# Kernel tuning notes

Measured on AMD Instinct MI355X. Metric: run time of the kernel, lower is better.

Reference implementation:

```python
import jax, jax.numpy as jnp
import numpy as np

DIM = 768
N_HEADS = 12
HEAD_DIM = DIM // N_HEADS
SCALE = HEAD_DIM ** -0.5


def setup_inputs() -> dict:
    key = jax.random.key(0)
    ks = jax.random.split(key, 5)
    B, N = 8, 1024
    x = jax.random.normal(ks[0], (B, N, DIM), dtype=jnp.float32)
    # Linear weights stored as (in, out) for x @ W; torch stores (out, in).
    w_qkv = jax.random.normal(ks[1], (DIM, 3 * DIM), dtype=jnp.float32) * (DIM ** -0.5)
    b_qkv = jnp.zeros((3 * DIM,), dtype=jnp.float32)
    w_proj = jax.random.normal(ks[2], (DIM, DIM), dtype=jnp.float32) * (DIM ** -0.5)
    b_proj = jnp.zeros((DIM,), dtype=jnp.float32)
    return {"x": x, "w_qkv": w_qkv, "b_qkv": b_qkv, "w_proj": w_proj, "b_proj": b_proj}


def reference(x, w_qkv, b_qkv, w_proj, b_proj):
    B, N, _ = x.shape
    qkv = x @ w_qkv + b_qkv                       # [B, N, 3*dim]
    qkv = qkv.reshape(B, N, 3, N_HEADS, HEAD_DIM)
    qkv = jnp.transpose(qkv, (2, 0, 3, 1, 4))     # [3, B, H, N, hd]
    q, k, v = qkv[0], qkv[1], qkv[2]
    attn = jnp.einsum("bhqd,bhkd->bhqk", q, k) * SCALE
    attn = jax.nn.softmax(attn, axis=-1)
    out = jnp.einsum("bhqk,bhkd->bhqd", attn, v)  # [B, H, N, hd]
    out = jnp.transpose(out, (0, 2, 1, 3)).reshape(B, N, DIM)
    return out @ w_proj + b_proj
```

## Files before the change

kernel.cpp:

```cpp
#include <hip/hip_runtime.h>
#include <cstdint>

#define DIM 768
#define NH 12
#define HD 64
#define SEQ 1024
#define NBH 96

#define QOFF  ((size_t)0)
#define KOFF  ((size_t)6291456)
#define VOFF  ((size_t)12582912)
#define AOFF  ((size_t)18874368)
#define XOFF  ((size_t)25165824)
#define WQOFF ((size_t)31457280)
#define WPOFF ((size_t)33226752)

#define QSCALE 0.18033688f

#define WAIT_VM0   __builtin_amdgcn_s_waitcnt(0x0F70)
#define BAR        __builtin_amdgcn_s_barrier()
#define CFENCE     __asm__ __volatile__("" ::: "memory")

typedef __attribute__((ext_vector_type(8))) __bf16 bf16x8;
typedef __attribute__((ext_vector_type(2))) __bf16 bf16x2;
typedef __attribute__((ext_vector_type(4))) float f32x4;
typedef __attribute__((ext_vector_type(4))) short s16x4;
typedef unsigned short u16;

__device__ __forceinline__ u16 f2bf(float f) {
    union { float f; unsigned u; } x; x.f = f;
    unsigned r = x.u + 0x7fffu + ((x.u >> 16) & 1u);
    return (u16)(r >> 16);
}

__device__ __forceinline__ unsigned pkbf(float a, float b) {
#if __has_builtin(__builtin_amdgcn_cvt_pk_bf16_f32)
    bf16x2 v = __builtin_amdgcn_cvt_pk_bf16_f32(a, b);
    union { bf16x2 v; unsigned u; } c; c.v = v; return c.u;
#else
    return (unsigned)f2bf(a) | ((unsigned)f2bf(b) << 16);
#endif
}

__device__ __forceinline__ void async_cp16(const void* g, void* l) {
    __builtin_amdgcn_global_load_lds((const __attribute__((address_space(1))) void*)g,
                                     (__attribute__((address_space(3))) void*)l, 16, 0, 0);
}

__global__ __launch_bounds__(256) void prep(const float* __restrict__ x,
                                            const float* __restrict__ wq,
                                            const float* __restrict__ wp,
                                            u16* __restrict__ ws) {
    const int bid = blockIdx.x;
    const int tid = threadIdx.x;
    if (bid < 3072) {
        size_t i = (size_t)bid * 512 + tid;
#pragma unroll
        for (int j = 0; j < 2; ++j, i += 256) {
            float4 v = *(const float4*)&x[i * 4];
            ushort4 o;
            o.x = f2bf(v.x); o.y = f2bf(v.y); o.z = f2bf(v.z); o.w = f2bf(v.w);
            *(ushort4*)&ws[XOFF + i * 4] = o;
        }
        return;
    }
    __shared__ float T[64][65];
    const float* w; u16* wt; int N, bx, by;
    if (bid < 3504) { int b = bid - 3072; w = wq; wt = ws + WQOFF; N = 2304; bx = b % 36; by = b / 36; }
    else            { int b = bid - 3504; w = wp; wt = ws + WPOFF; N = 768;  bx = b % 12; by = b / 12; }
    const int K = 768;
    const int k0 = by * 64, n0 = bx * 64;
    const int r = tid >> 4, c4 = (tid & 15) * 4;
#pragma unroll
    for (int i = 0; i < 4; ++i) {
        float4 v = *(const float4*)&w[(size_t)(k0 + r + 16 * i) * N + n0 + c4];
        T[r + 16 * i][c4 + 0] = v.x; T[r + 16 * i][c4 + 1] = v.y;
        T[r + 16 * i][c4 + 2] = v.z; T[r + 16 * i][c4 + 3] = v.w;
    }
    __syncthreads();
#pragma unroll
    for (int i = 0; i < 4; ++i) {
        int rr = r + 16 * i;
        ushort4 o;
        o.x = f2bf(T[c4 + 0][rr]); o.y = f2bf(T[c4 + 1][rr]);
        o.z = f2bf(T[c4 + 2][rr]); o.w = f2bf(T[c4 + 3][rr]);
        *(ushort4*)&wt[(size_t)(n0 + rr) * K + k0 + c4] = o;
    }
}

template <int EPI, int NC>
__global__ __launch_bounds__(256, 3) void gemm_bt(const u16* __restrict__ A,
                                                  const u16* __restrict__ Bt,
                                                  const float* __restrict__ bias,
                                                  float* __restrict__ outf,
                                                  u16* __restrict__ outq) {
    __shared__ __align__(16) u16 As[128 * 64];
    __shared__ __align__(16) u16 Bs[32 * NC * 64];
    const int tid = threadIdx.x;
    const int lane = tid & 63;
    const int w = tid >> 6;
    const int wm = w >> 1, wn = w & 1;
    const int m0 = blockIdx.y * 128, n0 = blockIdx.x * (32 * NC);

    const int lgrp = lane >> 3;
    const int gg = (lane & 7) ^ lgrp;
    const u16* ga = A  + (size_t)(m0 + w * 32 + lgrp) * 768 + gg * 8;
    const u16* gb = Bt + (size_t)(n0 + w * 8 * NC + lgrp) * 768 + gg * 8;
    u16* lba = As + w * 32 * 64;
    u16* lbb = Bs + w * 8 * NC * 64;

    const int l15 = lane & 15, qg = lane >> 4, q4 = qg * 4;

    int aoff[4][2], boff[NC][2];
#pragma unroll
    for (int r = 0; r < 4; ++r) {
        int row = 64 * wm + 16 * r + l15;
#pragma unroll
        for (int kc = 0; kc < 2; ++kc)
            aoff[r][kc] = row * 64 + (((4 * kc + qg) ^ (row & 7)) << 3);
    }
#pragma unroll
    for (int c = 0; c < NC; ++c) {
        int row = 16 * NC * wn + 16 * c + l15;
#pragma unroll
        for (int kc = 0; kc < 2; ++kc)
            boff[c][kc] = row * 64 + (((4 * kc + qg) ^ (row & 7)) << 3);
    }

    f32x4 acc[4][NC] = {};

    for (int k0 = 0; k0 < 768; k0 += 64) {
#pragma unroll
        for (int i = 0; i < 4; ++i)
            async_cp16(ga + (size_t)i * 8 * 768 + k0, lba + i * 512);
#pragma unroll
        for (int i = 0; i < NC; ++i)
            async_cp16(gb + (size_t)i * 8 * 768 + k0, lbb + i * 512);
        __syncthreads();
#pragma unroll
        for (int kc = 0; kc < 2; ++kc) {
            bf16x8 af[4], bfr[NC];
#pragma unroll
            for (int r = 0; r < 4; ++r) af[r] = *(const bf16x8*)&As[aoff[r][kc]];
#pragma unroll
            for (int c = 0; c < NC; ++c) bfr[c] = *(const bf16x8*)&Bs[boff[c][kc]];
#pragma unroll
            for (int r = 0; r < 4; ++r)
#pragma unroll
                for (int c = 0; c < NC; ++c)
                    acc[r][c] = __builtin_amdgcn_mfma_f32_16x16x32_bf16(af[r], bfr[c], acc[r][c], 0, 0, 0);
        }
        __syncthreads();
    }

#pragma unroll
    for (int r = 0; r < 4; ++r) {
#pragma unroll
        for (int c = 0; c < NC; ++c) {
            const int cg = n0 + 16 * NC * wn + 16 * c + l15;
            const float bv = bias[cg];
            const int mb = m0 + 64 * wm + 16 * r + q4;
            if constexpr (EPI == 0) {
#pragma unroll
                for (int g = 0; g < 4; ++g)
                    outf[(size_t)(mb + g) * DIM + cg] = acc[r][c][g] + bv;
            } else {
                const int which = (cg >= 1536) ? 2 : (cg >= 768 ? 1 : 0);
                const int rem = cg - which * 768;
                const int h = rem >> 6, d = rem & 63;
                const int b = mb >> 10, q = mb & 1023;
                if (which == 0) {
#pragma unroll
                    for (int g = 0; g < 4; ++g)
                        outq[QOFF + ((size_t)(b * NH + h) * SEQ + q + g) * HD + d] =
                            f2bf((acc[r][c][g] + bv) * QSCALE);
                } else if (which == 1) {
#pragma unroll
                    for (int g = 0; g < 4; ++g)
                        outq[KOFF + ((size_t)(b * NH + h) * SEQ + q + g) * HD + d] =
                            f2bf(acc[r][c][g] + bv);
                } else {
                    ushort4 pk;
                    pk.x = f2bf(acc[r][c][0] + bv); pk.y = f2bf(acc[r][c][1] + bv);
                    pk.z = f2bf(acc[r][c][2] + bv); pk.w = f2bf(acc[r][c][3] + bv);
                    *(ushort4*)&outq[VOFF + ((size_t)(b * NH + h) * HD + d) * SEQ + q] = pk;
                }
            }
        }
    }
}

__global__ __launch_bounds__(256) void flash_attn(const u16* __restrict__ ws, u16* __restrict__ attn_out) {
    __shared__ __align__(16) u16 Ks[2][64 * 64];
    __shared__ __align__(16) u16 Vs[2][64 * 64];

    const int tid = threadIdx.x;
    const int lane = tid & 63;
    const int wv = tid >> 6;
    const int qt = blockIdx.x;
    const int bh = blockIdx.y;
    const u16* qp = ws + QOFF + (size_t)bh * SEQ * HD;
    const u16* kp = ws + KOFF + (size_t)bh * SEQ * HD;
    const u16* vp = ws + VOFF + (size_t)bh * HD * SEQ;

    const int l15 = lane & 15, qg = lane >> 4, q8 = qg * 8;
    const int l7 = l15 & 7;

    bf16x8 bq[2][2];
#pragma unroll
    for (int r = 0; r < 2; ++r)
#pragma unroll
        for (int kc = 0; kc < 2; ++kc)
            bq[r][kc] = *(const bf16x8*)&qp[(size_t)(qt * 128 + 32 * wv + 16 * r + l15) * HD + 32 * kc + q8];

    const int lgrp = lane >> 3;
    const int gg = (lane & 7) ^ lgrp;
    auto stage = [&](int buf, int ktv) {
#pragma unroll
        for (int i = 0; i < 2; ++i) {
            async_cp16(kp + (size_t)(ktv * 64 + wv * 16 + i * 8 + lgrp) * 64 + gg * 8,
                       &Ks[buf][(wv * 16 + i * 8) * 64]);
            async_cp16(vp + (size_t)(wv * 16 + i * 8 + lgrp) * SEQ + ktv * 64 + gg * 8,
                       &Vs[buf][(wv * 16 + i * 8) * 64]);
        }
    };
    stage(0, 0);

    int akoff[4][2], avoff[4][4];
#pragma unroll
    for (int c = 0; c < 4; ++c) {
#pragma unroll
        for (int kc = 0; kc < 2; ++kc)
            akoff[c][kc] = (16 * c + l15) * 64 + (((4 * kc + qg) ^ l7) << 3);
#pragma unroll
        for (int cd = 0; cd < 4; ++cd)
            avoff[c][cd] = (16 * cd + l15) * 64 + (((2 * c + (qg >> 1)) ^ l7) << 3) + (qg & 1) * 4;
    }

    f32x4 oacc[2][4] = {};
    float lsum[2] = {0.f, 0.f};

    for (int kt = 0; kt < 16; ++kt) {
        const int cur = kt & 1;
        WAIT_VM0;
        BAR;
        CFENCE;
        if (kt < 15) stage(cur ^ 1, kt + 1);

        f32x4 sacc[4][2] = {};
#pragma unroll
        for (int c = 0; c < 4; ++c) {
#pragma unroll
            for (int kc = 0; kc < 2; ++kc) {
                bf16x8 ak = *(const bf16x8*)&Ks[cur][akoff[c][kc]];
#pragma unroll
                for (int r = 0; r < 2; ++r)
                    sacc[c][r] = __builtin_amdgcn_mfma_f32_16x16x32_bf16(ak, bq[r][kc], sacc[c][r], 0, 0, 0);
            }
        }

        s16x4 pf[4][2];
#pragma unroll
        for (int c = 0; c < 4; ++c) {
#pragma unroll
            for (int r = 0; r < 2; ++r) {
                float p0 = __builtin_amdgcn_exp2f(sacc[c][r][0]);
                float p1 = __builtin_amdgcn_exp2f(sacc[c][r][1]);
                float p2 = __builtin_amdgcn_exp2f(sacc[c][r][2]);
                float p3 = __builtin_amdgcn_exp2f(sacc[c][r][3]);
                lsum[r] += (p0 + p1) + (p2 + p3);
                union { uint2 u; s16x4 v; } pk;
                pk.u.x = pkbf(p0, p1); pk.u.y = pkbf(p2, p3);
                pf[c][r] = pk.v;
            }
        }

#pragma unroll
        for (int c = 0; c < 4; ++c) {
            s16x4 av[4];
#pragma unroll
            for (int cd = 0; cd < 4; ++cd)
                av[cd] = *(const s16x4*)&Vs[cur][avoff[c][cd]];
#pragma unroll
            for (int r = 0; r < 2; ++r)
#pragma unroll
                for (int cd = 0; cd < 4; ++cd)
                    oacc[r][cd] = __builtin_amdgcn_mfma_f32_16x16x16bf16_1k(av[cd], pf[c][r], oacc[r][cd], 0, 0, 0);
        }
    }

#pragma unroll
    for (int r = 0; r < 2; ++r) {
        lsum[r] += __shfl_xor(lsum[r], 16);
        lsum[r] += __shfl_xor(lsum[r], 32);
    }

    const int b = bh / NH, h = bh % NH;
#pragma unroll
    for (int r = 0; r < 2; ++r) {
        const float inv = 1.f / lsum[r];
        const int qrow = qt * 128 + 32 * wv + 16 * r + l15;
        u16* orow = attn_out + (size_t)(b * SEQ + qrow) * DIM + h * HD + qg * 4;
#pragma unroll
        for (int cd = 0; cd < 4; ++cd) {
            ushort4 o;
            o.x = f2bf(oacc[r][cd][0] * inv); o.y = f2bf(oacc[r][cd][1] * inv);
            o.z = f2bf(oacc[r][cd][2] * inv); o.w = f2bf(oacc[r][cd][3] * inv);
            *(ushort4*)&orow[16 * cd] = o;
        }
    }
}

extern "C" void kernel_launch(void* const* d_in, const int* in_sizes, int n_in,
                              void* d_out, int out_size, void* d_ws, size_t ws_size,
                              hipStream_t stream) {
    const float* x      = (const float*)d_in[0];
    const float* w_qkv  = (const float*)d_in[1];
    const float* b_qkv  = (const float*)d_in[2];
    const float* w_proj = (const float*)d_in[3];
    const float* b_proj = (const float*)d_in[4];
    float* out = (float*)d_out;
    u16* ws = (u16*)d_ws;

    prep<<<3648, 256, 0, stream>>>(x, w_qkv, w_proj, ws);
    gemm_bt<1, 4><<<dim3(18, 64), 256, 0, stream>>>(ws + XOFF, ws + WQOFF, b_qkv, nullptr, ws);
    flash_attn<<<dim3(8, 96), 256, 0, stream>>>(ws, ws + AOFF);
    gemm_bt<0, 2><<<dim3(12, 64), 256, 0, stream>>>(ws + AOFF, ws + WPOFF, b_proj, out, nullptr);
}
```

Measured before the change: 195.4 us.

## Double-buffer GEMM tiles, remap block order for XCDs, add MFMA priority hints

The GEMM kernel now double-buffers its A/B shared-memory tiles, so global-to-LDS copies of the next K slice overlap with MFMA compute on the current one. This replaces the two barriers per iteration that serialised load and compute. Both the GEMM and flash-attention kernels remap the flat block index so that consecutive logical tiles land on the same XCD (stride-8 interleave), aiming for better L2 reuse of shared K/V and weight rows. The attention kernel also raises wave priority around its MFMA sections. The double buffers double LDS use in the GEMM, which may reduce occupancy under launch_bounds(256,3).

Result: slower. 201.7 us (+3.3%).

```diff
diff --git a/kernel.cpp b/kernel.cpp
--- a/kernel.cpp
+++ b/kernel.cpp
@@ -94,20 +94,24 @@
                                                   const float* __restrict__ bias,
                                                   float* __restrict__ outf,
                                                   u16* __restrict__ outq) {
-    __shared__ __align__(16) u16 As[128 * 64];
-    __shared__ __align__(16) u16 Bs[32 * NC * 64];
+    __shared__ __align__(16) u16 As[2][128 * 64];
+    __shared__ __align__(16) u16 Bs[2][32 * NC * 64];
     const int tid = threadIdx.x;
     const int lane = tid & 63;
     const int w = tid >> 6;
     const int wm = w >> 1, wn = w & 1;
-    const int m0 = blockIdx.y * 128, n0 = blockIdx.x * (32 * NC);
+
+    const int gx = gridDim.x;
+    const int flat = blockIdx.y * gx + blockIdx.x;
+    const int chunk = (gx * gridDim.y) >> 3;
+    const int nf = (flat & 7) * chunk + (flat >> 3);
+    const int bxs = nf % gx, bys = nf / gx;
+    const int m0 = bys * 128, n0 = bxs * (32 * NC);
 
     const int lgrp = lane >> 3;
     const int gg = (lane & 7) ^ lgrp;
     const u16* ga = A  + (size_t)(m0 + w * 32 + lgrp) * 768 + gg * 8;
     const u16* gb = Bt + (size_t)(n0 + w * 8 * NC + lgrp) * 768 + gg * 8;
-    u16* lba = As + w * 32 * 64;
-    u16* lbb = Bs + w * 8 * NC * 64;
 
     const int l15 = lane & 15, qg = lane >> 4, q4 = qg * 4;
 
@@ -129,28 +133,43 @@
 
     f32x4 acc[4][NC] = {};
 
-    for (int k0 = 0; k0 < 768; k0 += 64) {
+    auto stage = [&](int buf, int k0) {
 #pragma unroll
         for (int i = 0; i < 4; ++i)
-            async_cp16(ga + (size_t)i * 8 * 768 + k0, lba + i * 512);
+            async_cp16(ga + (size_t)i * 8 * 768 + k0, &As[buf][w * 32 * 64 + i * 512]);
 #pragma unroll
         for (int i = 0; i < NC; ++i)
-            async_cp16(gb + (size_t)i * 8 * 768 + k0, lbb + i * 512);
-        __syncthreads();
+            async_cp16(gb + (size_t)i * 8 * 768 + k0, &Bs[buf][w * 8 * NC * 64 + i * 512]);
+    };
+    auto compute = [&](const u16* Ab, const u16* Bb) {
 #pragma unroll
         for (int kc = 0; kc < 2; ++kc) {
             bf16x8 af[4], bfr[NC];
 #pragma unroll
-            for (int r = 0; r < 4; ++r) af[r] = *(const bf16x8*)&As[aoff[r][kc]];
-#pragma unroll
-            for (int c = 0; c < NC; ++c) bfr[c] = *(const bf16x8*)&Bs[boff[c][kc]];
+            for (int r = 0; r < 4; ++r) af[r] = *(const bf16x8*)&Ab[aoff[r][kc]];
+#pragma unroll
+            for (int c = 0; c < NC; ++c) bfr[c] = *(const bf16x8*)&Bb[boff[c][kc]];
 #pragma unroll
             for (int r = 0; r < 4; ++r)
 #pragma unroll
                 for (int c = 0; c < NC; ++c)
                     acc[r][c] = __builtin_amdgcn_mfma_f32_16x16x32_bf16(af[r], bfr[c], acc[r][c], 0, 0, 0);
         }
-        __syncthreads();
+    };
+
+    stage(0, 0);
+    for (int kt = 0; kt < 768; kt += 128) {
+        WAIT_VM0;
+        BAR;
+        CFENCE;
+        if (kt + 64 < 768) stage(1, kt + 64);
+        compute(&As[0][0], &Bs[0][0]);
+
+        WAIT_VM0;
+        BAR;
+        CFENCE;
+        if (kt + 128 < 768) stage(0, kt + 128);
+        compute(&As[1][0], &Bs[1][0]);
     }
 
 #pragma unroll
@@ -197,8 +216,12 @@
     const int tid = threadIdx.x;
     const int lane = tid & 63;
     const int wv = tid >> 6;
-    const int qt = blockIdx.x;
-    const int bh = blockIdx.y;
+
+    const int flat = blockIdx.y * 8 + blockIdx.x;
+    const int nf = (flat & 7) * 96 + (flat >> 3);
+    const int qt = nf & 7;
+    const int bh = nf >> 3;
+
     const u16* qp = ws + QOFF + (size_t)bh * SEQ * HD;
     const u16* kp = ws + KOFF + (size_t)bh * SEQ * HD;
     const u16* vp = ws + VOFF + (size_t)bh * HD * SEQ;
@@ -247,6 +270,7 @@
         CFENCE;
         if (kt < 15) stage(cur ^ 1, kt + 1);
 
+        __builtin_amdgcn_s_setprio(1);
         f32x4 sacc[4][2] = {};
 #pragma unroll
         for (int c = 0; c < 4; ++c) {
@@ -258,6 +282,7 @@
                     sacc[c][r] = __builtin_amdgcn_mfma_f32_16x16x32_bf16(ak, bq[r][kc], sacc[c][r], 0, 0, 0);
             }
         }
+        __builtin_amdgcn_s_setprio(0);
 
         s16x4 pf[4][2];
 #pragma unroll
@@ -275,6 +300,7 @@
             }
         }
 
+        __builtin_amdgcn_s_setprio(1);
 #pragma unroll
         for (int c = 0; c < 4; ++c) {
             s16x4 av[4];
@@ -287,6 +313,7 @@
                 for (int cd = 0; cd < 4; ++cd)
                     oacc[r][cd] = __builtin_amdgcn_mfma_f32_16x16x16bf16_1k(av[cd], pf[c][r], oacc[r][cd], 0, 0, 0);
         }
+        __builtin_amdgcn_s_setprio(0);
     }
 
 #pragma unroll
```
